# Optimization experiments

Hardware: AMD Instinct MI355X
Metric: run time of the kernel (lower is better)

## Reference

```python
import jax, jax.numpy as jnp
import numpy as np

B, T, E = 2, 2048, 2048
H, H_KV, D = 16, 8, 128
THETA = 10000.0


def setup_inputs() -> dict:
    key = jax.random.key(0)
    ks = jax.random.split(key, 5)
    s = lambda n: (1.0 / np.sqrt(n))
    x = jax.random.normal(ks[0], (B, T, E), dtype=jnp.float32)
    wq = jax.random.normal(ks[1], (E, H * D), dtype=jnp.float32) * s(E)
    wk = jax.random.normal(ks[2], (E, H_KV * D), dtype=jnp.float32) * s(E)
    wv = jax.random.normal(ks[3], (E, H_KV * D), dtype=jnp.float32) * s(E)
    wo = jax.random.normal(ks[4], (H * D, E), dtype=jnp.float32) * s(H * D)
    # causal mask, broadcast over batch and heads
    mask = jnp.tril(jnp.ones((T, T), dtype=jnp.int32))[None, None, :, :]
    return {"x": x, "mask": mask, "wq": wq, "wk": wk, "wv": wv, "wo": wo}


def _rope(q, k):
    # q,k: [B,H,T,D]; deinterleave even/odd, rotate, concat halves (as in source)
    Tq, Dh = q.shape[2], q.shape[3] // 2
    inv = 1.0 / (THETA ** (jnp.arange(Dh, dtype=jnp.float32) / Dh))
    ang = jnp.arange(Tq, dtype=jnp.float32)[:, None] * inv[None, :]  # [T,Dh]
    c, s = jnp.cos(ang), jnp.sin(ang)  # broadcast over [B,H]
    q1, q2 = q[..., ::2], q[..., 1::2]
    k1, k2 = k[..., ::2], k[..., 1::2]
    q_rot = jnp.concatenate([q1 * c - q2 * s, q2 * c + q1 * s], axis=-1)
    k_rot = jnp.concatenate([k1 * c - k2 * s, k2 * c + k1 * s], axis=-1)
    return q_rot, k_rot


def reference(x, mask, wq, wk, wv, wo):
    Bx, Tx, _ = x.shape
    scale = D ** -0.5
    q = (x @ wq).reshape(Bx, Tx, H, D).transpose(0, 2, 1, 3)      # [B,H,T,D]
    k = (x @ wk).reshape(Bx, Tx, H_KV, D).transpose(0, 2, 1, 3)   # [B,Hkv,T,D]
    v = (x @ wv).reshape(Bx, Tx, H_KV, D).transpose(0, 2, 1, 3)
    # torch .repeat tiles along head axis: [kv0..kv7, kv0..kv7]
    k = jnp.tile(k, (1, H // H_KV, 1, 1))
    v = jnp.tile(v, (1, H // H_KV, 1, 1))
    q, k = _rope(q, k)
    attn = jnp.einsum('bhtd,bhsd->bhts', q, k) * scale
    attn = jnp.where(mask == 0, -jnp.inf, attn)
    w = jax.nn.softmax(attn, axis=-1)
    w = jnp.where(jnp.isnan(w), 0.0, w)
    out = jnp.einsum('bhts,bhsd->bhtd', w, v)
    out = out.transpose(0, 2, 1, 3).reshape(Bx, Tx, H * D)
    return out @ wo
```

## Files before the change

kernel.cpp:

```cpp
#include <hip/hip_runtime.h>
#include <hip/hip_bf16.h>
#include <cstdint>

typedef short bf16x8 __attribute__((ext_vector_type(8)));
typedef float f32x4 __attribute__((ext_vector_type(4)));
typedef unsigned short u16;
typedef unsigned int u32;

#define TT 2048

__device__ __forceinline__ u16 f2bf(float f) {
    __hip_bfloat16 h = __float2bfloat16(f);
    return __builtin_bit_cast(u16, h);
}
__device__ __forceinline__ float bf2f(u16 u) {
    return __builtin_bit_cast(float, (u32)u << 16);
}
__device__ __forceinline__ f32x4 mfma16(bf16x8 a, bf16x8 b, f32x4 c) {
    return __builtin_amdgcn_mfma_f32_16x16x32_bf16(a, b, c, 0, 0, 0);
}
__device__ __forceinline__ bf16x8 ldg8(const u16* p) {
    return __builtin_bit_cast(bf16x8, *reinterpret_cast<const uint4*>(p));
}
__device__ __forceinline__ bf16x8 lds8(const u16* p) {
    return *reinterpret_cast<const bf16x8*>(p);
}
__device__ __forceinline__ void gll16(const u16* g, u16* l) {
    __builtin_amdgcn_global_load_lds(
        (const __attribute__((address_space(1))) void*)g,
        (__attribute__((address_space(3))) void*)l, 16, 0, 0);
}

__global__ __launch_bounds__(256) void prologue(const float* __restrict__ x,
                                                const float* __restrict__ wq,
                                                const float* __restrict__ wk,
                                                const float* __restrict__ wv,
                                                const float* __restrict__ wo,
                                                u16* __restrict__ xb,
                                                u16* __restrict__ wqkvT,
                                                u16* __restrict__ woT) {
    const int z = blockIdx.z;
    const int tid = threadIdx.x;
    if (z == 4) {
        int bix = blockIdx.y * 32 + blockIdx.x;
#pragma unroll
        for (int k = 0; k < 4; k++) {
            int idx = (bix * 1024 + k * 256 + tid) * 8;
            float4 a = *reinterpret_cast<const float4*>(&x[idx]);
            float4 b = *reinterpret_cast<const float4*>(&x[idx + 4]);
            u16 o[8] = {f2bf(a.x), f2bf(a.y), f2bf(a.z), f2bf(a.w),
                        f2bf(b.x), f2bf(b.y), f2bf(b.z), f2bf(b.w)};
            *reinterpret_cast<uint4*>(&xb[idx]) = *reinterpret_cast<const uint4*>(o);
        }
        return;
    }
    const float* src;
    u16* dst;
    int C, rope;
    const int R = 2048;
    if (z == 0) { src = wq; dst = wqkvT;               C = 2048; rope = 1; }
    else if (z == 1) { src = wk; dst = wqkvT + 2048 * 2048; C = 1024; rope = 1; }
    else if (z == 2) { src = wv; dst = wqkvT + 3072 * 2048; C = 1024; rope = 0; }
    else { src = wo; dst = woT;                        C = 2048; rope = 0; }
    const int cb = blockIdx.x, rb = blockIdx.y;
    if (cb * 64 >= C) return;

    __shared__ float tl[64][65];
#pragma unroll
    for (int i = 0; i < 16; i++) {
        int li = i * 256 + tid;
        int tr = li >> 6, tc = li & 63;
        tl[tr][tc] = src[(size_t)(rb * 64 + tr) * C + cb * 64 + tc];
    }
    __syncthreads();
#pragma unroll
    for (int i = 0; i < 16; i++) {
        int li = i * 256 + tid;
        int dr = li >> 6, dc = li & 63;
        int c = cb * 64 + dr;
        int j;
        if (rope) {
            int head = c >> 7, cl = c & 127, ii = cl >> 1, odd = cl & 1;
            j = head * 128 + ((ii & 15) | (odd << 4) | ((ii >> 4) << 5));
        } else {
            j = c;
        }
        dst[(size_t)j * R + rb * 64 + dc] = f2bf(tl[dc][dr]);
    }
}

template <int MODE>
__global__ __launch_bounds__(256) void gemm_bt(const u16* __restrict__ A,
                                               const u16* __restrict__ BT,
                                               void* __restrict__ P0, void* __restrict__ P1,
                                               void* __restrict__ P2, int M, int N, int K) {
    __shared__ __align__(16) u16 smA[2][128 * 64];
    __shared__ __align__(16) u16 smB[2][128 * 64];
    const int tid = threadIdx.x;
    const int w = tid >> 6, lane = tid & 63, quad = lane >> 4, l15 = lane & 15;
    const int wr = w >> 1, wc = w & 1;
    const int bm = blockIdx.y, bn = blockIdx.x;

    f32x4 acc[4][4];
    const f32x4 zf = {0.f, 0.f, 0.f, 0.f};
#pragma unroll
    for (int i = 0; i < 4; i++)
#pragma unroll
        for (int j = 0; j < 4; j++) acc[i][j] = zf;

    const u16* aSrc[4];
    const u16* bSrc[4];
#pragma unroll
    for (int i = 0; i < 4; i++) {
        int o = i * 256 + tid;
        int r = o >> 3, p = o & 7;
        int cc = p ^ (r & 7);
        aSrc[i] = A + (size_t)(bm * 128 + r) * K + cc * 8;
        bSrc[i] = BT + (size_t)(bn * 128 + r) * K + cc * 8;
    }
    auto stage = [&](int buf) {
#pragma unroll
        for (int i = 0; i < 4; i++) {
            gll16(aSrc[i], &smA[buf][(i * 256 + w * 64) * 8]);
            gll16(bSrc[i], &smB[buf][(i * 256 + w * 64) * 8]);
            aSrc[i] += 64;
            bSrc[i] += 64;
        }
    };

    stage(0);
    const int nkt = K >> 6;
    for (int kt = 0; kt < nkt; ++kt) {
        const int cur = kt & 1;
        __syncthreads();
        if (kt + 1 < nkt) stage(cur ^ 1);
#pragma unroll
        for (int ks = 0; ks < 2; ++ks) {
            const int cd = ks * 4 + quad;
            bf16x8 af[4], bf[4];
#pragma unroll
            for (int mi = 0; mi < 4; mi++) {
                int row = wr * 64 + mi * 16 + l15;
                af[mi] = lds8(&smA[cur][row * 64 + (cd ^ (row & 7)) * 8]);
            }
#pragma unroll
            for (int ni = 0; ni < 4; ni++) {
                int row = wc * 64 + ni * 16 + l15;
                bf[ni] = lds8(&smB[cur][row * 64 + (cd ^ (row & 7)) * 8]);
            }
#pragma unroll
            for (int mi = 0; mi < 4; mi++)
#pragma unroll
                for (int ni = 0; ni < 4; ni++) acc[mi][ni] = mfma16(af[mi], bf[ni], acc[mi][ni]);
        }
    }

    if (MODE == 1) {
#pragma unroll
        for (int mi = 0; mi < 4; mi++)
#pragma unroll
            for (int ni = 0; ni < 4; ni++)
#pragma unroll
                for (int r = 0; r < 4; r++) {
                    int m = bm * 128 + wr * 64 + mi * 16 + quad * 4 + r;
                    int n = bn * 128 + wc * 64 + ni * 16 + l15;
                    ((float*)P0)[(size_t)m * N + n] = acc[mi][ni][r];
                }
    } else if (bn < 24) {
#pragma unroll
        for (int mi = 0; mi < 4; mi++)
#pragma unroll
            for (int g = 0; g < 2; g++) {
                int i = (wc * 2 + g) * 16 + l15;
                float inv = __expf(-0.14391156644f * (float)i);
#pragma unroll
                for (int r = 0; r < 4; r++) {
                    int m = bm * 128 + wr * 64 + mi * 16 + quad * 4 + r;
                    int b = m >> 11, t = m & 2047;
                    float ang = (float)t * inv;
                    float sn, cs;
                    __sincosf(ang, &sn, &cs);
                    float x1 = acc[mi][2 * g][r], x2 = acc[mi][2 * g + 1][r];
                    u16 o1 = f2bf(x1 * cs - x2 * sn);
                    u16 o2 = f2bf(x2 * cs + x1 * sn);
                    if (bn < 16) {
                        u16* pq = (u16*)P0 + ((size_t)(b * 16 + bn) * 2048 + t) * 128;
                        pq[i] = o1;
                        pq[i + 64] = o2;
                    } else {
                        u16* pk = (u16*)P1 + ((size_t)(b * 8 + (bn - 16)) * 2048 + t) * 128;
                        pk[i] = o1;
                        pk[i + 64] = o2;
                    }
                }
            }
    } else {
#pragma unroll
        for (int mi = 0; mi < 4; mi++)
#pragma unroll
            for (int ni = 0; ni < 4; ni++)
#pragma unroll
                for (int r = 0; r < 4; r++) {
                    int m = bm * 128 + wr * 64 + mi * 16 + quad * 4 + r;
                    int b = m >> 11, t = m & 2047;
                    int d = wc * 64 + ni * 16 + l15;
                    int h = bn - 24;
                    ((u16*)P2)[((size_t)(b * 8 + h) * 128 + d) * 2048 + t] =
                        f2bf(acc[mi][ni][r]);
                }
    }
}

__global__ __launch_bounds__(256) void flash_attn(const u16* __restrict__ qg,
                                                  const u16* __restrict__ kg,
                                                  const u16* __restrict__ vg,
                                                  u16* __restrict__ og) {
    __shared__ __align__(16) u16 Ksm[2][64 * 128];
    __shared__ __align__(16) u16 Vsm[2][128 * 64];
    __shared__ __align__(16) u16 Pt[4 * 32 * 64];
    const int tid = threadIdx.x, w = tid >> 6, lane = tid & 63, quad = lane >> 4,
              l15 = lane & 15;
    const int bkv = blockIdx.x;
    const int qblk = 31 - (int)blockIdx.y;
    const int b = bkv >> 3, kvh = bkv & 7;
    const float scale = 0.08838834764831845f;

    const u16* kb = kg + (size_t)(b * 8 + kvh) * 2048 * 128;
    const u16* vb = vg + (size_t)(b * 8 + kvh) * 128 * 2048;

    bf16x8 aq[2][4];
#pragma unroll
    for (int hh = 0; hh < 2; hh++) {
        const int h = kvh + hh * 8;
        const u16* qp =
            qg + ((size_t)(b * 16 + h) * 2048 + qblk * 64 + w * 16 + l15) * 128 + quad * 8;
#pragma unroll
        for (int kk = 0; kk < 4; kk++) aq[hh][kk] = ldg8(qp + kk * 32);
    }

    f32x4 oacc[2][8];
    f32x4 lacc[2];
    const f32x4 zf = {0.f, 0.f, 0.f, 0.f};
#pragma unroll
    for (int hh = 0; hh < 2; hh++) {
        lacc[hh] = zf;
#pragma unroll
        for (int j = 0; j < 8; j++) oacc[hh][j] = zf;
    }
    bf16x8 ones;
#pragma unroll
    for (int i = 0; i < 8; i++) ones[i] = (short)0x3F80;

    auto stage = [&](int st, int buf) {
#pragma unroll
        for (int i = 0; i < 4; i++) {
            int o = i * 256 + w * 64 + lane;
            int s = o >> 4, p = o & 15;
            int cc = (p & 8) | ((p ^ s) & 7);
            gll16(kb + (size_t)(st * 64 + s) * 128 + cc * 8, &Ksm[buf][(i * 256 + w * 64) * 8]);
            int d = o >> 3, p2 = o & 7;
            int cc2 = (p2 ^ d) & 7;
            gll16(vb + (size_t)d * 2048 + st * 64 + cc2 * 8, &Vsm[buf][(i * 256 + w * 64) * 8]);
        }
    };

    stage(0, 0);
    for (int st = 0; st <= qblk; ++st) {
        const int cur = st & 1;
        __syncthreads();
        if (st < qblk) stage(st + 1, cur ^ 1);

        f32x4 s0[4], s1[4];
#pragma unroll
        for (int j = 0; j < 4; j++) {
            s0[j] = zf;
            s1[j] = zf;
#pragma unroll
            for (int kk = 0; kk < 4; kk++) {
                int srow = j * 16 + l15;
                int cd = kk * 4 + quad;
                int p = (cd & 8) | ((cd ^ srow) & 7);
                bf16x8 bk = lds8(&Ksm[cur][srow * 128 + p * 8]);
                s0[j] = mfma16(aq[0][kk], bk, s0[j]);
                s1[j] = mfma16(aq[1][kk], bk, s1[j]);
            }
        }
        const bool diag = (st == qblk);
#pragma unroll
        for (int j = 0; j < 4; j++)
#pragma unroll
            for (int r = 0; r < 4; r++) {
                bool masked = diag && (j * 16 + l15) > (w * 16 + quad * 4 + r);
                float p0 = masked ? 0.f : __expf(s0[j][r] * scale);
                float p1 = masked ? 0.f : __expf(s1[j][r] * scale);
                int prow = w * 32 + quad * 4 + r;
                int cc = (j * 2 + (l15 >> 3));
                int off = (l15 & 7);
                Pt[prow * 64 + ((cc ^ (prow & 7)) * 8) + off] = f2bf(p0);
                int prow1 = prow + 16;
                Pt[prow1 * 64 + ((cc ^ (prow1 & 7)) * 8) + off] = f2bf(p1);
            }
#pragma unroll
        for (int kk = 0; kk < 2; kk++) {
            int row0 = w * 32 + l15, row1 = row0 + 16;
            int cd2 = kk * 4 + quad;
            bf16x8 ap0 = lds8(&Pt[row0 * 64 + ((cd2 ^ (row0 & 7)) * 8)]);
            bf16x8 ap1 = lds8(&Pt[row1 * 64 + ((cd2 ^ (row1 & 7)) * 8)]);
#pragma unroll
            for (int jf = 0; jf < 8; jf++) {
                int drow = jf * 16 + l15;
                int p2 = (cd2 ^ drow) & 7;
                bf16x8 bv = lds8(&Vsm[cur][drow * 64 + p2 * 8]);
                oacc[0][jf] = mfma16(ap0, bv, oacc[0][jf]);
                oacc[1][jf] = mfma16(ap1, bv, oacc[1][jf]);
            }
            lacc[0] = mfma16(ap0, ones, lacc[0]);
            lacc[1] = mfma16(ap1, ones, lacc[1]);
        }
    }
#pragma unroll
    for (int hh = 0; hh < 2; hh++) {
        const int h = kvh + hh * 8;
#pragma unroll
        for (int jf = 0; jf < 8; jf++)
#pragma unroll
            for (int r = 0; r < 4; r++) {
                int t = qblk * 64 + w * 16 + quad * 4 + r;
                int d = jf * 16 + l15;
                og[((size_t)(b * 2048 + t) * 16 + h) * 128 + d] =
                    f2bf(oacc[hh][jf][r] / lacc[hh][r]);
            }
    }
}

extern "C" void kernel_launch(void* const* d_in, const int* in_sizes, int n_in, void* d_out,
                              int out_size, void* d_ws, size_t ws_size, hipStream_t stream) {
    const float* x = (const float*)d_in[0];
    const float* wq = (const float*)d_in[2];
    const float* wk = (const float*)d_in[3];
    const float* wv = (const float*)d_in[4];
    const float* wo = (const float*)d_in[5];
    float* out = (float*)d_out;

    char* ws = (char*)d_ws;
    u16* xb = (u16*)(ws);
    u16* wqkvT = (u16*)(ws + 16777216);
    u16* woT = (u16*)(ws + 33554432);
    u16* qbuf = (u16*)(ws + 41943040);
    u16* kbuf = (u16*)(ws + 58720256);
    u16* vtb = (u16*)(ws + 67108864);
    u16* obuf = xb;

    prologue<<<dim3(32, 32, 5), 256, 0, stream>>>(x, wq, wk, wv, wo, xb, wqkvT, woT);

    gemm_bt<0><<<dim3(32, 32), 256, 0, stream>>>(xb, wqkvT, qbuf, kbuf, vtb, 4096, 4096, 2048);

    flash_attn<<<dim3(16, 32), 256, 0, stream>>>(qbuf, kbuf, vtb, obuf);

    gemm_bt<1><<<dim3(16, 32), 256, 0, stream>>>(obuf, woT, out, nullptr, nullptr, 4096, 2048,
                                                 2048);
}
```

Measured before the change: 313.4 us.

## Use 256x256 GEMM tiles with 8 waves and interleaved LDS/MFMA schedule

Replaces the 128x128, 4-wave GEMM with a 256x256, 8-wave kernel used for both the QKV and output projections. Each wave computes 128x64 in four quadrant phases, with explicit barriers, s_setprio around the MFMA bursts, and a two-deep global_load_lds prefetch driven by manual vmcnt waits. The aim is more data reuse per LDS byte and better overlap of loads with MFMA work. The output GEMM now launches only 128 blocks, which may leave CUs idle. The larger per-wave accumulator also raises register pressure, and the hand-written waitcnt logic is easy to get wrong.

```diff
diff --git a/kernel.cpp b/kernel.cpp
--- a/kernel.cpp
+++ b/kernel.cpp
@@ -30,6 +30,11 @@
         (const __attribute__((address_space(1))) void*)g,
         (__attribute__((address_space(3))) void*)l, 16, 0, 0);
 }
+
+#define ASMBAR asm volatile("s_barrier" ::: "memory")
+#define WAIT_VM8 asm volatile("s_waitcnt vmcnt(8)" ::: "memory")
+#define WAIT_VM0 asm volatile("s_waitcnt vmcnt(0)" ::: "memory")
+#define WAIT_LGKM0 asm volatile("s_waitcnt lgkmcnt(0)" ::: "memory")
 
 __global__ __launch_bounds__(256) void prologue(const float* __restrict__ x,
                                                 const float* __restrict__ wq,
@@ -90,21 +95,21 @@
 }
 
 template <int MODE>
-__global__ __launch_bounds__(256) void gemm_bt(const u16* __restrict__ A,
-                                               const u16* __restrict__ BT,
-                                               void* __restrict__ P0, void* __restrict__ P1,
-                                               void* __restrict__ P2, int M, int N, int K) {
-    __shared__ __align__(16) u16 smA[2][128 * 64];
-    __shared__ __align__(16) u16 smB[2][128 * 64];
+__global__ __launch_bounds__(512, 2) void gemm256(const u16* __restrict__ A,
+                                                  const u16* __restrict__ BT,
+                                                  void* __restrict__ P0, void* __restrict__ P1,
+                                                  void* __restrict__ P2, int M, int N, int K) {
+    __shared__ __align__(16) u16 smA[2][256 * 64];
+    __shared__ __align__(16) u16 smB[2][256 * 64];
     const int tid = threadIdx.x;
     const int w = tid >> 6, lane = tid & 63, quad = lane >> 4, l15 = lane & 15;
-    const int wr = w >> 1, wc = w & 1;
+    const int wr = w >> 2, wc = w & 3;
     const int bm = blockIdx.y, bn = blockIdx.x;
 
-    f32x4 acc[4][4];
+    f32x4 acc[8][4];
     const f32x4 zf = {0.f, 0.f, 0.f, 0.f};
 #pragma unroll
-    for (int i = 0; i < 4; i++)
+    for (int i = 0; i < 8; i++)
 #pragma unroll
         for (int j = 0; j < 4; j++) acc[i][j] = zf;
 
@@ -112,70 +117,133 @@
     const u16* bSrc[4];
 #pragma unroll
     for (int i = 0; i < 4; i++) {
-        int o = i * 256 + tid;
+        int o = i * 512 + tid;
         int r = o >> 3, p = o & 7;
         int cc = p ^ (r & 7);
-        aSrc[i] = A + (size_t)(bm * 128 + r) * K + cc * 8;
-        bSrc[i] = BT + (size_t)(bn * 128 + r) * K + cc * 8;
+        aSrc[i] = A + (size_t)(bm * 256 + r) * K + cc * 8;
+        bSrc[i] = BT + (size_t)(bn * 256 + r) * K + cc * 8;
     }
     auto stage = [&](int buf) {
 #pragma unroll
         for (int i = 0; i < 4; i++) {
-            gll16(aSrc[i], &smA[buf][(i * 256 + w * 64) * 8]);
-            gll16(bSrc[i], &smB[buf][(i * 256 + w * 64) * 8]);
+            gll16(aSrc[i], &smA[buf][(i * 512 + w * 64) * 8]);
             aSrc[i] += 64;
+        }
+#pragma unroll
+        for (int i = 0; i < 4; i++) {
+            gll16(bSrc[i], &smB[buf][(i * 512 + w * 64) * 8]);
             bSrc[i] += 64;
         }
     };
 
     stage(0);
+    stage(1);
+    WAIT_VM8;
+    ASMBAR;
+
     const int nkt = K >> 6;
     for (int kt = 0; kt < nkt; ++kt) {
         const int cur = kt & 1;
-        __syncthreads();
-        if (kt + 1 < nkt) stage(cur ^ 1);
-#pragma unroll
-        for (int ks = 0; ks < 2; ++ks) {
-            const int cd = ks * 4 + quad;
-            bf16x8 af[4], bf[4];
-#pragma unroll
-            for (int mi = 0; mi < 4; mi++) {
-                int row = wr * 64 + mi * 16 + l15;
-                af[mi] = lds8(&smA[cur][row * 64 + (cd ^ (row & 7)) * 8]);
-            }
-#pragma unroll
-            for (int ni = 0; ni < 4; ni++) {
-                int row = wc * 64 + ni * 16 + l15;
-                bf[ni] = lds8(&smB[cur][row * 64 + (cd ^ (row & 7)) * 8]);
-            }
-#pragma unroll
-            for (int mi = 0; mi < 4; mi++)
-#pragma unroll
-                for (int ni = 0; ni < 4; ni++) acc[mi][ni] = mfma16(af[mi], bf[ni], acc[mi][ni]);
-        }
+        bf16x8 a[4][2], b01[2][2], b23[2][2];
+#pragma unroll
+        for (int mi = 0; mi < 4; mi++)
+#pragma unroll
+            for (int ks = 0; ks < 2; ks++) {
+                int row = wr * 128 + mi * 16 + l15, cd = ks * 4 + quad;
+                a[mi][ks] = lds8(&smA[cur][row * 64 + ((cd ^ (row & 7)) * 8)]);
+            }
+#pragma unroll
+        for (int ni = 0; ni < 2; ni++)
+#pragma unroll
+            for (int ks = 0; ks < 2; ks++) {
+                int row = wc * 64 + ni * 16 + l15, cd = ks * 4 + quad;
+                b01[ni][ks] = lds8(&smB[cur][row * 64 + ((cd ^ (row & 7)) * 8)]);
+            }
+        ASMBAR;
+        __builtin_amdgcn_s_setprio(1);
+#pragma unroll
+        for (int mi = 0; mi < 4; mi++)
+#pragma unroll
+            for (int ni = 0; ni < 2; ni++)
+#pragma unroll
+                for (int ks = 0; ks < 2; ks++)
+                    acc[mi][ni] = mfma16(a[mi][ks], b01[ni][ks], acc[mi][ni]);
+        __builtin_amdgcn_s_setprio(0);
+        ASMBAR;
+#pragma unroll
+        for (int ni = 0; ni < 2; ni++)
+#pragma unroll
+            for (int ks = 0; ks < 2; ks++) {
+                int row = wc * 64 + (ni + 2) * 16 + l15, cd = ks * 4 + quad;
+                b23[ni][ks] = lds8(&smB[cur][row * 64 + ((cd ^ (row & 7)) * 8)]);
+            }
+        ASMBAR;
+        __builtin_amdgcn_s_setprio(1);
+#pragma unroll
+        for (int mi = 0; mi < 4; mi++)
+#pragma unroll
+            for (int ni = 0; ni < 2; ni++)
+#pragma unroll
+                for (int ks = 0; ks < 2; ks++)
+                    acc[mi][ni + 2] = mfma16(a[mi][ks], b23[ni][ks], acc[mi][ni + 2]);
+        __builtin_amdgcn_s_setprio(0);
+        ASMBAR;
+#pragma unroll
+        for (int mi = 0; mi < 4; mi++)
+#pragma unroll
+            for (int ks = 0; ks < 2; ks++) {
+                int row = wr * 128 + (mi + 4) * 16 + l15, cd = ks * 4 + quad;
+                a[mi][ks] = lds8(&smA[cur][row * 64 + ((cd ^ (row & 7)) * 8)]);
+            }
+        ASMBAR;
+        __builtin_amdgcn_s_setprio(1);
+#pragma unroll
+        for (int mi = 0; mi < 4; mi++)
+#pragma unroll
+            for (int ni = 0; ni < 2; ni++)
+#pragma unroll
+                for (int ks = 0; ks < 2; ks++)
+                    acc[mi + 4][ni + 2] = mfma16(a[mi][ks], b23[ni][ks], acc[mi + 4][ni + 2]);
+        __builtin_amdgcn_s_setprio(0);
+        WAIT_LGKM0;
+        ASMBAR;
+        if (kt + 2 < nkt) stage(cur);
+        ASMBAR;
+        __builtin_amdgcn_s_setprio(1);
+#pragma unroll
+        for (int mi = 0; mi < 4; mi++)
+#pragma unroll
+            for (int ni = 0; ni < 2; ni++)
+#pragma unroll
+                for (int ks = 0; ks < 2; ks++)
+                    acc[mi + 4][ni] = mfma16(a[mi][ks], b01[ni][ks], acc[mi + 4][ni]);
+        __builtin_amdgcn_s_setprio(0);
+        if (kt + 2 < nkt) { WAIT_VM8; }
+        else if (kt + 1 < nkt) { WAIT_VM0; }
+        ASMBAR;
     }
 
     if (MODE == 1) {
 #pragma unroll
-        for (int mi = 0; mi < 4; mi++)
+        for (int mi = 0; mi < 8; mi++)
 #pragma unroll
             for (int ni = 0; ni < 4; ni++)
 #pragma unroll
                 for (int r = 0; r < 4; r++) {
-                    int m = bm * 128 + wr * 64 + mi * 16 + quad * 4 + r;
-                    int n = bn * 128 + wc * 64 + ni * 16 + l15;
+                    int m = bm * 256 + wr * 128 + mi * 16 + quad * 4 + r;
+                    int n = bn * 256 + wc * 64 + ni * 16 + l15;
                     ((float*)P0)[(size_t)m * N + n] = acc[mi][ni][r];
                 }
-    } else if (bn < 24) {
-#pragma unroll
-        for (int mi = 0; mi < 4; mi++)
+    } else if (bn < 12) {
+#pragma unroll
+        for (int mi = 0; mi < 8; mi++)
 #pragma unroll
             for (int g = 0; g < 2; g++) {
-                int i = (wc * 2 + g) * 16 + l15;
+                int i = ((wc & 1) * 2 + g) * 16 + l15;
                 float inv = __expf(-0.14391156644f * (float)i);
 #pragma unroll
                 for (int r = 0; r < 4; r++) {
-                    int m = bm * 128 + wr * 64 + mi * 16 + quad * 4 + r;
+                    int m = bm * 256 + wr * 128 + mi * 16 + quad * 4 + r;
                     int b = m >> 11, t = m & 2047;
                     float ang = (float)t * inv;
                     float sn, cs;
@@ -183,12 +251,14 @@
                     float x1 = acc[mi][2 * g][r], x2 = acc[mi][2 * g + 1][r];
                     u16 o1 = f2bf(x1 * cs - x2 * sn);
                     u16 o2 = f2bf(x2 * cs + x1 * sn);
-                    if (bn < 16) {
-                        u16* pq = (u16*)P0 + ((size_t)(b * 16 + bn) * 2048 + t) * 128;
+                    if (bn < 8) {
+                        int h = bn * 2 + (wc >> 1);
+                        u16* pq = (u16*)P0 + ((size_t)(b * 16 + h) * 2048 + t) * 128;
                         pq[i] = o1;
                         pq[i + 64] = o2;
                     } else {
-                        u16* pk = (u16*)P1 + ((size_t)(b * 8 + (bn - 16)) * 2048 + t) * 128;
+                        int hk = (bn - 8) * 2 + (wc >> 1);
+                        u16* pk = (u16*)P1 + ((size_t)(b * 8 + hk) * 2048 + t) * 128;
                         pk[i] = o1;
                         pk[i + 64] = o2;
                     }
@@ -196,15 +266,15 @@
             }
     } else {
 #pragma unroll
-        for (int mi = 0; mi < 4; mi++)
+        for (int mi = 0; mi < 8; mi++)
 #pragma unroll
             for (int ni = 0; ni < 4; ni++)
 #pragma unroll
                 for (int r = 0; r < 4; r++) {
-                    int m = bm * 128 + wr * 64 + mi * 16 + quad * 4 + r;
+                    int m = bm * 256 + wr * 128 + mi * 16 + quad * 4 + r;
                     int b = m >> 11, t = m & 2047;
-                    int d = wc * 64 + ni * 16 + l15;
-                    int h = bn - 24;
+                    int d = (wc & 1) * 64 + ni * 16 + l15;
+                    int h = (bn - 12) * 2 + (wc >> 1);
                     ((u16*)P2)[((size_t)(b * 8 + h) * 128 + d) * 2048 + t] =
                         f2bf(acc[mi][ni][r]);
                 }
@@ -353,10 +423,10 @@
 
     prologue<<<dim3(32, 32, 5), 256, 0, stream>>>(x, wq, wk, wv, wo, xb, wqkvT, woT);
 
-    gemm_bt<0><<<dim3(32, 32), 256, 0, stream>>>(xb, wqkvT, qbuf, kbuf, vtb, 4096, 4096, 2048);
+    gemm256<0><<<dim3(16, 16), 512, 0, stream>>>(xb, wqkvT, qbuf, kbuf, vtb, 4096, 4096, 2048);
 
     flash_attn<<<dim3(16, 32), 256, 0, stream>>>(qbuf, kbuf, vtb, obuf);
 
-    gemm_bt<1><<<dim3(16, 32), 256, 0, stream>>>(obuf, woT, out, nullptr, nullptr, 4096, 2048,
-                                                 2048);
-}
+    gemm256<1><<<dim3(8, 16), 512, 0, stream>>>(obuf, woT, out, nullptr, nullptr, 4096, 2048,
+                                                2048);
+}
```

New measurement: 341.5 us. 1.09x slower.

## Rewrite QKV GEMM as 256x256 8-wave ping-pong pipelined kernel; vectorize prologue stores

Applied to the files above, without the earlier changes.

Replaces the 128x128 QKV projection GEMM with a 512-thread, 256x256-tile kernel. It interleaves LDS fragment reads, global-to-LDS staging and MFMA batches, using explicit barriers, waitcnt and setprio to overlap memory with compute. The RoPE and V-transpose epilogue indices are remapped to the larger tile. The prologue weight transpose now writes 8 bf16 values per 16-byte store instead of scalar stores, and the output projection keeps the old GEMM as a separate kernel. The manual synchronisation is fragile, and the larger tile halves the block count, which lowers parallelism across CUs.

```diff
diff --git a/kernel.cpp b/kernel.cpp
--- a/kernel.cpp
+++ b/kernel.cpp
@@ -30,6 +30,11 @@
         (const __attribute__((address_space(1))) void*)g,
         (__attribute__((address_space(3))) void*)l, 16, 0, 0);
 }
+
+#define ASMBAR asm volatile("s_barrier" ::: "memory")
+#define WAIT_VM4 asm volatile("s_waitcnt vmcnt(4)" ::: "memory")
+#define WAIT_VM0 asm volatile("s_waitcnt vmcnt(0)" ::: "memory")
+#define WAIT_LGKM0 asm volatile("s_waitcnt lgkmcnt(0)" ::: "memory")
 
 __global__ __launch_bounds__(256) void prologue(const float* __restrict__ x,
                                                 const float* __restrict__ wq,
@@ -74,9 +79,9 @@
     }
     __syncthreads();
 #pragma unroll
-    for (int i = 0; i < 16; i++) {
-        int li = i * 256 + tid;
-        int dr = li >> 6, dc = li & 63;
+    for (int i = 0; i < 2; i++) {
+        int task = i * 256 + tid;
+        int dr = task >> 3, dc0 = (task & 7) * 8;
         int c = cb * 64 + dr;
         int j;
         if (rope) {
@@ -85,97 +90,138 @@
         } else {
             j = c;
         }
-        dst[(size_t)j * R + rb * 64 + dc] = f2bf(tl[dc][dr]);
-    }
-}
-
-template <int MODE>
-__global__ __launch_bounds__(256) void gemm_bt(const u16* __restrict__ A,
-                                               const u16* __restrict__ BT,
-                                               void* __restrict__ P0, void* __restrict__ P1,
-                                               void* __restrict__ P2, int M, int N, int K) {
-    __shared__ __align__(16) u16 smA[2][128 * 64];
-    __shared__ __align__(16) u16 smB[2][128 * 64];
+        u16 o[8];
+#pragma unroll
+        for (int k2 = 0; k2 < 8; k2++) o[k2] = f2bf(tl[dc0 + k2][dr]);
+        *reinterpret_cast<uint4*>(&dst[(size_t)j * R + rb * 64 + dc0]) =
+            *reinterpret_cast<const uint4*>(o);
+    }
+}
+
+__global__ __launch_bounds__(512, 2) void gemm8p(const u16* __restrict__ A,
+                                                 const u16* __restrict__ BT,
+                                                 u16* __restrict__ Pq, u16* __restrict__ Pk,
+                                                 u16* __restrict__ Pv, int M, int N, int K) {
+    __shared__ __align__(16) u16 smA[2][256 * 64];
+    __shared__ __align__(16) u16 smB[2][256 * 64];
     const int tid = threadIdx.x;
     const int w = tid >> 6, lane = tid & 63, quad = lane >> 4, l15 = lane & 15;
-    const int wr = w >> 1, wc = w & 1;
+    const int wr = w >> 2, wc = w & 3;
     const int bm = blockIdx.y, bn = blockIdx.x;
 
-    f32x4 acc[4][4];
+    f32x4 acc[8][4];
     const f32x4 zf = {0.f, 0.f, 0.f, 0.f};
 #pragma unroll
-    for (int i = 0; i < 4; i++)
+    for (int i = 0; i < 8; i++)
 #pragma unroll
         for (int j = 0; j < 4; j++) acc[i][j] = zf;
 
-    const u16* aSrc[4];
-    const u16* bSrc[4];
-#pragma unroll
-    for (int i = 0; i < 4; i++) {
-        int o = i * 256 + tid;
-        int r = o >> 3, p = o & 7;
-        int cc = p ^ (r & 7);
-        aSrc[i] = A + (size_t)(bm * 128 + r) * K + cc * 8;
-        bSrc[i] = BT + (size_t)(bn * 128 + r) * K + cc * 8;
-    }
-    auto stage = [&](int buf) {
-#pragma unroll
-        for (int i = 0; i < 4; i++) {
-            gll16(aSrc[i], &smA[buf][(i * 256 + w * 64) * 8]);
-            gll16(bSrc[i], &smB[buf][(i * 256 + w * 64) * 8]);
-            aSrc[i] += 64;
-            bSrc[i] += 64;
-        }
-    };
-
-    stage(0);
-    const int nkt = K >> 6;
-    for (int kt = 0; kt < nkt; ++kt) {
-        const int cur = kt & 1;
-        __syncthreads();
-        if (kt + 1 < nkt) stage(cur ^ 1);
-#pragma unroll
-        for (int ks = 0; ks < 2; ++ks) {
-            const int cd = ks * 4 + quad;
-            bf16x8 af[4], bf[4];
-#pragma unroll
-            for (int mi = 0; mi < 4; mi++) {
-                int row = wr * 64 + mi * 16 + l15;
-                af[mi] = lds8(&smA[cur][row * 64 + (cd ^ (row & 7)) * 8]);
-            }
-#pragma unroll
-            for (int ni = 0; ni < 4; ni++) {
-                int row = wc * 64 + ni * 16 + l15;
-                bf[ni] = lds8(&smB[cur][row * 64 + (cd ^ (row & 7)) * 8]);
-            }
-#pragma unroll
-            for (int mi = 0; mi < 4; mi++)
-#pragma unroll
-                for (int ni = 0; ni < 4; ni++) acc[mi][ni] = mfma16(af[mi], bf[ni], acc[mi][ni]);
-        }
-    }
-
-    if (MODE == 1) {
+    const int r0 = tid >> 3;
+    const int cc0 = (tid & 7) ^ (r0 & 7);
+    const u16* aSrc = A + (size_t)(bm * 256 + r0) * K + cc0 * 8;
+    const u16* bSrc = BT + (size_t)(bn * 256 + r0) * K + cc0 * 8;
+    auto stageA = [&](int buf, int kt) {
+#pragma unroll
+        for (int i = 0; i < 4; i++)
+            gll16(aSrc + (size_t)i * 64 * K + kt * 64, &smA[buf][(i * 512 + w * 64) * 8]);
+    };
+    auto stageB = [&](int buf, int kt) {
+#pragma unroll
+        for (int i = 0; i < 4; i++)
+            gll16(bSrc + (size_t)i * 64 * K + kt * 64, &smB[buf][(i * 512 + w * 64) * 8]);
+    };
+    bf16x8 aL[4][2], aH[4][2], b01e[2][2], b01o[2][2], b23[2][2];
+    auto rdA4 = [&](bf16x8(&dst)[4][2], int c, int mo) {
 #pragma unroll
         for (int mi = 0; mi < 4; mi++)
 #pragma unroll
-            for (int ni = 0; ni < 4; ni++)
+            for (int ks = 0; ks < 2; ks++) {
+                int row = wr * 128 + (mo + mi) * 16 + l15, cd = ks * 4 + quad;
+                dst[mi][ks] = lds8(&smA[c][row * 64 + ((cd ^ (row & 7)) * 8)]);
+            }
+    };
+    auto rdB2 = [&](bf16x8(&dst)[2][2], int c, int no) {
+#pragma unroll
+        for (int ni = 0; ni < 2; ni++)
+#pragma unroll
+            for (int ks = 0; ks < 2; ks++) {
+                int row = wc * 64 + (no + ni) * 16 + l15, cd = ks * 4 + quad;
+                dst[ni][ks] = lds8(&smB[c][row * 64 + ((cd ^ (row & 7)) * 8)]);
+            }
+    };
+    auto mfma8x = [&](bf16x8(&af)[4][2], bf16x8(&bf)[2][2], int mo, int no) {
+        __builtin_amdgcn_s_setprio(1);
+#pragma unroll
+        for (int mi = 0; mi < 4; mi++)
+#pragma unroll
+            for (int ni = 0; ni < 2; ni++)
+#pragma unroll
+                for (int ks = 0; ks < 2; ks++)
+                    acc[mo + mi][no + ni] =
+                        mfma16(af[mi][ks], bf[ni][ks], acc[mo + mi][no + ni]);
+        __builtin_amdgcn_s_setprio(0);
+    };
+
+    stageA(0, 0);
+    stageB(0, 0);
+    stageA(1, 1);
+    WAIT_VM4;
+    ASMBAR;
+    rdA4(aL, 0, 0);
+    rdB2(b01e, 0, 0);
+
+    const int nkt = K >> 6, niter = nkt >> 1;
+    for (int it = 0; it < niter; ++it) {
+        const bool more = it + 1 < niter;
+        const int t1 = 2 * it + 1, t2 = 2 * it + 2, t3 = 2 * it + 3;
+        rdB2(b23, 0, 2);
+        stageB(1, t1);
+        ASMBAR;
+        mfma8x(aL, b01e, 0, 0);
+        rdA4(aH, 0, 4);
+        ASMBAR;
+        mfma8x(aL, b23, 0, 2);
+        ASMBAR;
+        mfma8x(aH, b23, 4, 2);
+        WAIT_LGKM0;
+        WAIT_VM0;
+        ASMBAR;
+        rdA4(aL, 1, 0);
+        rdB2(b01o, 1, 0);
+        if (more) stageA(0, t2);
+        ASMBAR;
+        mfma8x(aH, b01e, 4, 0);
+        rdB2(b23, 1, 2);
+        if (more) stageB(0, t2);
+        ASMBAR;
+        mfma8x(aL, b01o, 0, 0);
+        rdA4(aH, 1, 4);
+        ASMBAR;
+        mfma8x(aL, b23, 0, 2);
+        ASMBAR;
+        mfma8x(aH, b23, 4, 2);
+        WAIT_LGKM0;
+        if (more) WAIT_VM0;
+        ASMBAR;
+        if (more) {
+            rdA4(aL, 0, 0);
+            rdB2(b01e, 0, 0);
+            stageA(1, t3);
+        }
+        ASMBAR;
+        mfma8x(aH, b01o, 4, 0);
+    }
+
+    if (bn < 12) {
+#pragma unroll
+        for (int mi = 0; mi < 8; mi++)
+#pragma unroll
+            for (int g = 0; g < 2; g++) {
+                int i = ((wc & 1) * 2 + g) * 16 + l15;
+                float inv = __expf(-0.14391156644f * (float)i);
 #pragma unroll
                 for (int r = 0; r < 4; r++) {
-                    int m = bm * 128 + wr * 64 + mi * 16 + quad * 4 + r;
-                    int n = bn * 128 + wc * 64 + ni * 16 + l15;
-                    ((float*)P0)[(size_t)m * N + n] = acc[mi][ni][r];
-                }
-    } else if (bn < 24) {
-#pragma unroll
-        for (int mi = 0; mi < 4; mi++)
-#pragma unroll
-            for (int g = 0; g < 2; g++) {
-                int i = (wc * 2 + g) * 16 + l15;
-                float inv = __expf(-0.14391156644f * (float)i);
-#pragma unroll
-                for (int r = 0; r < 4; r++) {
-                    int m = bm * 128 + wr * 64 + mi * 16 + quad * 4 + r;
+                    int m = bm * 256 + wr * 128 + mi * 16 + quad * 4 + r;
                     int b = m >> 11, t = m & 2047;
                     float ang = (float)t * inv;
                     float sn, cs;
@@ -183,12 +229,14 @@
                     float x1 = acc[mi][2 * g][r], x2 = acc[mi][2 * g + 1][r];
                     u16 o1 = f2bf(x1 * cs - x2 * sn);
                     u16 o2 = f2bf(x2 * cs + x1 * sn);
-                    if (bn < 16) {
-                        u16* pq = (u16*)P0 + ((size_t)(b * 16 + bn) * 2048 + t) * 128;
+                    if (bn < 8) {
+                        int h = bn * 2 + (wc >> 1);
+                        u16* pq = Pq + ((size_t)(b * 16 + h) * 2048 + t) * 128;
                         pq[i] = o1;
                         pq[i + 64] = o2;
                     } else {
-                        u16* pk = (u16*)P1 + ((size_t)(b * 8 + (bn - 16)) * 2048 + t) * 128;
+                        int hk = (bn - 8) * 2 + (wc >> 1);
+                        u16* pk = Pk + ((size_t)(b * 8 + hk) * 2048 + t) * 128;
                         pk[i] = o1;
                         pk[i + 64] = o2;
                     }
@@ -196,19 +244,94 @@
             }
     } else {
 #pragma unroll
-        for (int mi = 0; mi < 4; mi++)
+        for (int mi = 0; mi < 8; mi++)
 #pragma unroll
             for (int ni = 0; ni < 4; ni++)
 #pragma unroll
                 for (int r = 0; r < 4; r++) {
-                    int m = bm * 128 + wr * 64 + mi * 16 + quad * 4 + r;
+                    int m = bm * 256 + wr * 128 + mi * 16 + quad * 4 + r;
                     int b = m >> 11, t = m & 2047;
-                    int d = wc * 64 + ni * 16 + l15;
-                    int h = bn - 24;
-                    ((u16*)P2)[((size_t)(b * 8 + h) * 128 + d) * 2048 + t] =
-                        f2bf(acc[mi][ni][r]);
+                    int d = (wc & 1) * 64 + ni * 16 + l15;
+                    int h = (bn - 12) * 2 + (wc >> 1);
+                    Pv[((size_t)(b * 8 + h) * 128 + d) * 2048 + t] = f2bf(acc[mi][ni][r]);
                 }
     }
+}
+
+__global__ __launch_bounds__(256) void gemm_o(const u16* __restrict__ A,
+                                              const u16* __restrict__ BT,
+                                              float* __restrict__ C, int M, int N, int K) {
+    __shared__ __align__(16) u16 smA[2][128 * 64];
+    __shared__ __align__(16) u16 smB[2][128 * 64];
+    const int tid = threadIdx.x;
+    const int w = tid >> 6, lane = tid & 63, quad = lane >> 4, l15 = lane & 15;
+    const int wr = w >> 1, wc = w & 1;
+    const int bm = blockIdx.y, bn = blockIdx.x;
+
+    f32x4 acc[4][4];
+    const f32x4 zf = {0.f, 0.f, 0.f, 0.f};
+#pragma unroll
+    for (int i = 0; i < 4; i++)
+#pragma unroll
+        for (int j = 0; j < 4; j++) acc[i][j] = zf;
+
+    const u16* aSrc[4];
+    const u16* bSrc[4];
+#pragma unroll
+    for (int i = 0; i < 4; i++) {
+        int o = i * 256 + tid;
+        int r = o >> 3, p = o & 7;
+        int cc = p ^ (r & 7);
+        aSrc[i] = A + (size_t)(bm * 128 + r) * K + cc * 8;
+        bSrc[i] = BT + (size_t)(bn * 128 + r) * K + cc * 8;
+    }
+    auto stage = [&](int buf) {
+#pragma unroll
+        for (int i = 0; i < 4; i++) {
+            gll16(aSrc[i], &smA[buf][(i * 256 + w * 64) * 8]);
+            gll16(bSrc[i], &smB[buf][(i * 256 + w * 64) * 8]);
+            aSrc[i] += 64;
+            bSrc[i] += 64;
+        }
+    };
+
+    stage(0);
+    const int nkt = K >> 6;
+    for (int kt = 0; kt < nkt; ++kt) {
+        const int cur = kt & 1;
+        __syncthreads();
+        if (kt + 1 < nkt) stage(cur ^ 1);
+#pragma unroll
+        for (int ks = 0; ks < 2; ++ks) {
+            const int cd = ks * 4 + quad;
+            bf16x8 af[4], bf[4];
+#pragma unroll
+            for (int mi = 0; mi < 4; mi++) {
+                int row = wr * 64 + mi * 16 + l15;
+                af[mi] = lds8(&smA[cur][row * 64 + (cd ^ (row & 7)) * 8]);
+            }
+#pragma unroll
+            for (int ni = 0; ni < 4; ni++) {
+                int row = wc * 64 + ni * 16 + l15;
+                bf[ni] = lds8(&smB[cur][row * 64 + (cd ^ (row & 7)) * 8]);
+            }
+#pragma unroll
+            for (int mi = 0; mi < 4; mi++)
+#pragma unroll
+                for (int ni = 0; ni < 4; ni++) acc[mi][ni] = mfma16(af[mi], bf[ni], acc[mi][ni]);
+        }
+    }
+
+#pragma unroll
+    for (int mi = 0; mi < 4; mi++)
+#pragma unroll
+        for (int ni = 0; ni < 4; ni++)
+#pragma unroll
+            for (int r = 0; r < 4; r++) {
+                int m = bm * 128 + wr * 64 + mi * 16 + quad * 4 + r;
+                int n = bn * 128 + wc * 64 + ni * 16 + l15;
+                C[(size_t)m * N + n] = acc[mi][ni][r];
+            }
 }
 
 __global__ __launch_bounds__(256) void flash_attn(const u16* __restrict__ qg,
@@ -353,10 +476,9 @@
 
     prologue<<<dim3(32, 32, 5), 256, 0, stream>>>(x, wq, wk, wv, wo, xb, wqkvT, woT);
 
-    gemm_bt<0><<<dim3(32, 32), 256, 0, stream>>>(xb, wqkvT, qbuf, kbuf, vtb, 4096, 4096, 2048);
+    gemm8p<<<dim3(16, 16), 512, 0, stream>>>(xb, wqkvT, qbuf, kbuf, vtb, 4096, 4096, 2048);
 
     flash_attn<<<dim3(16, 32), 256, 0, stream>>>(qbuf, kbuf, vtb, obuf);
 
-    gemm_bt<1><<<dim3(16, 32), 256, 0, stream>>>(obuf, woT, out, nullptr, nullptr, 4096, 2048,
-                                                 2048);
-}
+    gemm_o<<<dim3(16, 32), 256, 0, stream>>>(obuf, woT, out, 4096, 2048, 2048);
+}
```

Result: slower. 391.5 us (+24.9%).
